# Kernel tuning notes

Hardware: AMD Instinct MI355X
Metric: run time of the kernel (lower is better)

## Reference

```python
import jax, jax.numpy as jnp
import numpy as np

B, S, D = 2, 2048, 1024   # batch, seq, d_model
L, H = 256, 512           # d_latent, d_hidden (expert MLP)
E = 8                     # num_experts
SH = 512                  # shared-expert hidden (= d_hidden)


def setup_inputs() -> dict:
    key = jax.random.key(0)
    ks = jax.random.split(key, 12)
    s = 0.02
    return {
        "x": jax.random.normal(ks[0], (B, S, D), dtype=jnp.float32),
        "w_router": jax.random.normal(ks[1], (E, D), dtype=jnp.float32) * s,
        "w_down": jax.random.normal(ks[2], (L, D), dtype=jnp.float32) * s,
        "w_up": jax.random.normal(ks[3], (D, L), dtype=jnp.float32) * s,
        "w1_e": jax.random.normal(ks[4], (E, H, L), dtype=jnp.float32) * s,
        "wg_e": jax.random.normal(ks[5], (E, H, L), dtype=jnp.float32) * s,
        "w2_e": jax.random.normal(ks[6], (E, L, H), dtype=jnp.float32) * s,
        "w1_s": jax.random.normal(ks[7], (SH, D), dtype=jnp.float32) * s,
        "wg_s": jax.random.normal(ks[8], (SH, D), dtype=jnp.float32) * s,
        "w2_s": jax.random.normal(ks[9], (D, SH), dtype=jnp.float32) * s,
        "top_k": 2,
    }


def reference(x, w_router, w_down, w_up, w1_e, wg_e, w2_e, w1_s, wg_s, w2_s, top_k):
    Bq, Sq, Dq = x.shape
    T = Bq * Sq
    xf = x.reshape(T, Dq)

    # --- router (fp32 logits, softmax over top-k values) ---
    logits = xf.astype(jnp.float32) @ w_router.T            # (T, E)
    topk_val, topk_idx = jax.lax.top_k(logits, top_k)       # (T, k)
    topk_w = jax.nn.softmax(topk_val, axis=-1).astype(x.dtype)
    # dense combine weights (T, E); zero for unselected experts
    comb = jnp.zeros((T, E), dtype=x.dtype)
    comb = comb.at[jnp.arange(T)[:, None], topk_idx].add(topk_w)

    # --- shared latent down-projection ---
    lat = xf @ w_down.T                                     # (T, L)

    # --- all-expert SwiGLU in latent space, then weighted combine ---
    g = jax.nn.silu(jnp.einsum('tl,ehl->teh', lat, wg_e))   # (T, E, H)
    a = jnp.einsum('tl,ehl->teh', lat, w1_e)                # (T, E, H)
    ex = jnp.einsum('teh,elh->tel', g * a, w2_e)            # (T, E, L)
    routed_lat = jnp.einsum('te,tel->tl', comb, ex)         # (T, L)
    routed = routed_lat @ w_up.T                            # (T, D)

    # --- shared (dense) SwiGLU expert in d_model ---
    shared = (jax.nn.silu(xf @ wg_s.T) * (xf @ w1_s.T)) @ w2_s.T

    y = routed + shared
    return y.reshape(Bq, Sq, Dq)
```

## Files before the change

kernel.cpp:

```cpp
#include <hip/hip_runtime.h>
#include <hip/hip_bf16.h>
#include <math.h>

#define T_TOK 4096
#define D_MODEL 1024
#define L_LAT 256
#define H_HID 512
#define E_EXP 8
#define SH_HID 512
#define TOT_EROWS (2 * T_TOK)

typedef __bf16 bf16x8 __attribute__((ext_vector_type(8)));
typedef float f32x4 __attribute__((ext_vector_type(4)));

__device__ __forceinline__ unsigned short f2bf(float f) {
    union { float f; unsigned int u; } c{f};
    unsigned int r = (c.u + 0x7fffu + ((c.u >> 16) & 1u)) >> 16;
    return (unsigned short)r;
}
__device__ __forceinline__ float bf2f(unsigned short u) {
    union { unsigned int u; float f; } c{(unsigned int)u << 16};
    return c.f;
}

__device__ __forceinline__ void gload_lds16(const unsigned short* g, unsigned short* l) {
    __builtin_amdgcn_global_load_lds(
        (const __attribute__((address_space(1))) void*)g,
        (__attribute__((address_space(3))) void*)l,
        16, 0, 0);
}

__device__ __forceinline__ int swz64(int row, int s) {
    return s ^ (row & 7);
}

__global__ __launch_bounds__(256)
void cast_router_kernel(const float* __restrict__ x, const float* __restrict__ w_router,
                        const float* __restrict__ w_down, const float* __restrict__ wg_s,
                        const float* __restrict__ w1_s,
                        unsigned short* __restrict__ xb, unsigned short* __restrict__ wdb,
                        unsigned short* __restrict__ wgsb, unsigned short* __restrict__ w1sb,
                        int* __restrict__ topk_idx, float* __restrict__ topk_w)
{
    __shared__ float wlds[E_EXP * D_MODEL];
    int bid = blockIdx.x;
    int tid = threadIdx.x;

    if (bid < 4096) {
        int j = (bid * 256 + tid) * 4;
        float4 v = *(const float4*)(x + j);
        ushort4 o = { f2bf(v.x), f2bf(v.y), f2bf(v.z), f2bf(v.w) };
        *(ushort4*)(xb + j) = o;
        return;
    }
    if (bid >= 5120) {
        int i = (bid - 5120) * 256 + tid;
        const float* src; unsigned short* dst; int base;
        if      (i < 65536)  { src = w_down; dst = wdb;  base = 0; }
        else if (i < 196608) { src = wg_s;   dst = wgsb; base = 65536; }
        else                 { src = w1_s;   dst = w1sb; base = 196608; }
        int j = (i - base) * 4;
        float4 v = *(const float4*)(src + j);
        ushort4 o = { f2bf(v.x), f2bf(v.y), f2bf(v.z), f2bf(v.w) };
        *(ushort4*)(dst + j) = o;
        return;
    }

    int rb = bid - 4096;
    for (int i = tid * 4; i < E_EXP * D_MODEL; i += 256 * 4)
        *(float4*)(wlds + i) = *(const float4*)(w_router + i);
    __syncthreads();

    int wid = tid >> 6, lane = tid & 63;
    int t = rb * 4 + wid;
    const float* xr = x + (size_t)t * D_MODEL;
    float acc[E_EXP];
#pragma unroll
    for (int e = 0; e < E_EXP; ++e) acc[e] = 0.f;
#pragma unroll 4
    for (int i = 0; i < D_MODEL / 64; ++i) {
        int d = lane + i * 64;
        float xv = xr[d];
#pragma unroll
        for (int e = 0; e < E_EXP; ++e)
            acc[e] = fmaf(xv, wlds[e * D_MODEL + d], acc[e]);
    }
#pragma unroll
    for (int e = 0; e < E_EXP; ++e)
        for (int off = 32; off > 0; off >>= 1)
            acc[e] += __shfl_xor(acc[e], off, 64);
    if (lane == 0) {
        int i0 = 0; float v0 = acc[0];
#pragma unroll
        for (int e = 1; e < E_EXP; ++e) if (acc[e] > v0) { v0 = acc[e]; i0 = e; }
        int i1 = -1; float v1 = -INFINITY;
#pragma unroll
        for (int e = 0; e < E_EXP; ++e) if (e != i0 && acc[e] > v1) { v1 = acc[e]; i1 = e; }
        float e1 = expf(v1 - v0);
        topk_idx[2 * t] = i0; topk_idx[2 * t + 1] = i1;
        topk_w[2 * t] = 1.f / (1.f + e1);
        topk_w[2 * t + 1] = e1 / (1.f + e1);
    }
}

__device__ void bucket_body(const int* __restrict__ topk_idx,
                            int* __restrict__ counts, int* __restrict__ offsets,
                            int* __restrict__ tok_of_row, int* __restrict__ row_of_pair,
                            int* sb)
{
    int* s_wavecnt  = sb;
    int* s_wavebase = sb + 32;
    int* s_tot      = sb + 64;
    int* s_off      = sb + 72;
    int tid = threadIdx.x, wave = tid >> 6, lane = tid & 63;
    int base_i = tid * 32;

    int cnt[E_EXP];
#pragma unroll
    for (int e = 0; e < E_EXP; ++e) cnt[e] = 0;
#pragma unroll
    for (int j = 0; j < 32; ++j) {
        int e = topk_idx[base_i + j];
#pragma unroll
        for (int q = 0; q < E_EXP; ++q) cnt[q] += (e == q) ? 1 : 0;
    }
    int excl[E_EXP];
#pragma unroll
    for (int e = 0; e < E_EXP; ++e) {
        int v = cnt[e];
#pragma unroll
        for (int off = 1; off < 64; off <<= 1) {
            int u = __shfl_up(v, off, 64);
            v += (lane >= off) ? u : 0;
        }
        excl[e] = v - cnt[e];
        if (lane == 63) s_wavecnt[wave * 8 + e] = v;
    }
    __syncthreads();
    if (tid < E_EXP) {
        int tot = 0;
        for (int w = 0; w < 4; ++w) tot += s_wavecnt[w * 8 + tid];
        s_tot[tid] = tot;
        counts[tid] = tot;
    }
    __syncthreads();
    if (tid == 0) {
        int off = 0;
        for (int e = 0; e < E_EXP; ++e) { s_off[e] = off; offsets[e] = off; off += s_tot[e]; }
    }
    __syncthreads();
    if (tid < E_EXP) {
        int run = s_off[tid];
        for (int w = 0; w < 4; ++w) { s_wavebase[w * 8 + tid] = run; run += s_wavecnt[w * 8 + tid]; }
    }
    __syncthreads();
    int tb[E_EXP];
#pragma unroll
    for (int e = 0; e < E_EXP; ++e) tb[e] = s_wavebase[wave * 8 + e] + excl[e];
#pragma unroll
    for (int j = 0; j < 32; ++j) {
        int item = base_i + j;
        int e = topk_idx[item];
        int p = 0;
#pragma unroll
        for (int q = 0; q < E_EXP; ++q) if (e == q) { p = tb[q]; tb[q] = p + 1; }
        tok_of_row[p] = item >> 1;
        row_of_pair[item] = p;
    }
}

template<bool DUAL, bool SILU, bool EXPERT, bool GATHER, int OUT_MODE>
__device__ void gemm_tile(unsigned short* As, unsigned short* Bs0, unsigned short* Bs1,
                          int m0, int n0, int e,
                          const unsigned short* __restrict__ A,
                          const unsigned short* __restrict__ B0g,
                          const unsigned short* __restrict__ B1g,
                          void* __restrict__ Cv,
                          int M, int K, int ldc,
                          const int* __restrict__ tok_of_row,
                          const int* __restrict__ offsets,
                          const int* __restrict__ counts,
                          long strideB)
{
    int m_base = EXPERT ? offsets[e] : 0;
    int m_count = EXPERT ? counts[e] : M;
    if (m0 >= m_count) return;

    const unsigned short* B0 = B0g + (EXPERT ? (size_t)e * strideB : 0);
    const unsigned short* B1 = DUAL ? (B1g + (EXPERT ? (size_t)e * strideB : 0)) : nullptr;

    int tid = threadIdx.x;
    int r8 = tid >> 3, slot = tid & 7;

    const unsigned short* aptr[4];
#pragma unroll
    for (int r = 0; r < 4; ++r) {
        int rl = r * 32 + r8;
        int mrow = m0 + rl;
        if (mrow >= m_count) mrow = m_count - 1;
        long grow;
        if (GATHER)      grow = tok_of_row[m_base + mrow];
        else if (EXPERT) grow = m_base + mrow;
        else             grow = mrow;
        aptr[r] = A + (size_t)grow * K + swz64(rl, slot) * 8;
    }
    const unsigned short* bptr0[2];
    const unsigned short* bptr1[2];
#pragma unroll
    for (int r = 0; r < 2; ++r) {
        int rl = r * 32 + r8;
        int gs = swz64(rl, slot) * 8;
        bptr0[r] = B0 + (size_t)(n0 + rl) * K + gs;
        if (DUAL) bptr1[r] = B1 + (size_t)(n0 + rl) * K + gs;
    }
    unsigned short* As_dst  = As  + tid * 8;
    unsigned short* Bs0_dst = Bs0 + tid * 8;
    unsigned short* Bs1_dst = DUAL ? (Bs1 + tid * 8) : nullptr;

    int wave = tid >> 6, lane = tid & 63;
    int wm0 = (wave >> 1) * 64, wn0 = (wave & 1) * 32;
    int l15 = lane & 15, kg = lane >> 4;

    f32x4 acc0[4][2] = {};
    f32x4 acc1[DUAL ? 4 : 1][DUAL ? 2 : 1] = {};

    for (int k0 = 0; k0 < K; k0 += 64) {
#pragma unroll
        for (int r = 0; r < 4; ++r)
            gload_lds16(aptr[r] + k0, As_dst + r * 2048);
#pragma unroll
        for (int r = 0; r < 2; ++r) {
            gload_lds16(bptr0[r] + k0, Bs0_dst + r * 2048);
            if constexpr (DUAL) gload_lds16(bptr1[r] + k0, Bs1_dst + r * 2048);
        }
        __syncthreads();

        bf16x8 af[2][4];
#pragma unroll
        for (int kh = 0; kh < 2; ++kh)
#pragma unroll
            for (int mf = 0; mf < 4; ++mf) {
                int row = wm0 + mf * 16 + l15;
                af[kh][mf] = *reinterpret_cast<const bf16x8*>(As + row * 64 + swz64(row, kh * 4 + kg) * 8);
            }
        bf16x8 bf0[2][2], bf1[2][2];
#pragma unroll
        for (int kh = 0; kh < 2; ++kh)
#pragma unroll
            for (int nf = 0; nf < 2; ++nf) {
                int row = wn0 + nf * 16 + l15;
                bf0[kh][nf] = *reinterpret_cast<const bf16x8*>(Bs0 + row * 64 + swz64(row, kh * 4 + kg) * 8);
                if constexpr (DUAL)
                    bf1[kh][nf] = *reinterpret_cast<const bf16x8*>(Bs1 + row * 64 + swz64(row, kh * 4 + kg) * 8);
            }
#pragma unroll
        for (int kh = 0; kh < 2; ++kh)
#pragma unroll
            for (int mf = 0; mf < 4; ++mf)
#pragma unroll
                for (int nf = 0; nf < 2; ++nf) {
                    acc0[mf][nf] = __builtin_amdgcn_mfma_f32_16x16x32_bf16(af[kh][mf], bf0[kh][nf], acc0[mf][nf], 0, 0, 0);
                    if constexpr (DUAL)
                        acc1[mf][nf] = __builtin_amdgcn_mfma_f32_16x16x32_bf16(af[kh][mf], bf1[kh][nf], acc1[mf][nf], 0, 0, 0);
                }
        __syncthreads();
    }

#pragma unroll
    for (int mf = 0; mf < 4; ++mf) {
#pragma unroll
        for (int r4 = 0; r4 < 4; ++r4) {
            int mrow = m0 + wm0 + mf * 16 + kg * 4 + r4;
            if (mrow >= m_count) continue;
            size_t crow = (size_t)((EXPERT ? m_base : 0) + mrow) * ldc + n0 + wn0;
#pragma unroll
            for (int nf = 0; nf < 2; ++nf) {
                float v = acc0[mf][nf][r4];
                if constexpr (SILU) {
                    float g = v;
                    float a = acc1[mf][nf][r4];
                    v = (g / (1.f + expf(-g))) * a;
                }
                int col = nf * 16 + l15;
                if constexpr (OUT_MODE == 1) ((unsigned short*)Cv)[crow + col] = f2bf(v);
                else                         ((float*)Cv)[crow + col] = v;
            }
        }
    }
}

template<bool EXPERT, int OUT_MODE, bool BLEND>
__device__ void gemm_tile_n128(unsigned short* SM,
                               int m0, int n0, int e,
                               const unsigned short* __restrict__ A,
                               const unsigned short* __restrict__ B0g,
                               void* __restrict__ Cv,
                               int M, int K, int ldc,
                               const int* __restrict__ offsets,
                               const int* __restrict__ counts,
                               long strideB,
                               const int* __restrict__ row_of_pair,
                               const float* __restrict__ topk_w)
{
    unsigned short* As = SM;
    unsigned short* Bs = SM + 128 * 64;

    int m_base = EXPERT ? offsets[e] : 0;
    int m_count = EXPERT ? counts[e] : M;
    if (m0 >= m_count) return;

    const unsigned short* B0 = B0g + (EXPERT ? (size_t)e * strideB : 0);

    int tid = threadIdx.x;
    int r8 = tid >> 3, slot = tid & 7;

    const unsigned short* aptr[4];
    const unsigned short* a2ptr[4];
    float wa[4], wb[4];
#pragma unroll
    for (int r = 0; r < 4; ++r) {
        int rl = r * 32 + r8;
        int mrow = m0 + rl;
        if (mrow >= m_count) mrow = m_count - 1;
        if constexpr (BLEND) {
            int t = m0 + rl;
            int rp0 = row_of_pair[2 * t], rp1 = row_of_pair[2 * t + 1];
            wa[r] = topk_w[2 * t]; wb[r] = topk_w[2 * t + 1];
            aptr[r]  = A + (size_t)rp0 * K + swz64(rl, slot) * 8;
            a2ptr[r] = A + (size_t)rp1 * K + swz64(rl, slot) * 8;
        } else {
            long grow = EXPERT ? (long)(m_base + mrow) : (long)mrow;
            aptr[r] = A + (size_t)grow * K + swz64(rl, slot) * 8;
        }
    }
    const unsigned short* bptr[4];
#pragma unroll
    for (int r = 0; r < 4; ++r) {
        int rl = r * 32 + r8;
        bptr[r] = B0 + (size_t)(n0 + rl) * K + swz64(rl, slot) * 8;
    }
    unsigned short* As_dst = As + tid * 8;
    unsigned short* Bs_dst = Bs + tid * 8;

    int wave = tid >> 6, lane = tid & 63;
    int wm0 = (wave >> 1) * 64, wn0 = (wave & 1) * 64;
    int l15 = lane & 15, kg = lane >> 4;

    f32x4 acc[4][4] = {};

    for (int k0 = 0; k0 < K; k0 += 64) {
        if constexpr (BLEND) {
#pragma unroll
            for (int r = 0; r < 4; ++r) {
                ushort4 u0 = *(const ushort4*)(aptr[r] + k0);
                ushort4 u1 = *(const ushort4*)(aptr[r] + k0 + 4);
                ushort4 v0 = *(const ushort4*)(a2ptr[r] + k0);
                ushort4 v1 = *(const ushort4*)(a2ptr[r] + k0 + 4);
                ushort4 lo = { f2bf(wa[r] * bf2f(u0.x) + wb[r] * bf2f(v0.x)),
                               f2bf(wa[r] * bf2f(u0.y) + wb[r] * bf2f(v0.y)),
                               f2bf(wa[r] * bf2f(u0.z) + wb[r] * bf2f(v0.z)),
                               f2bf(wa[r] * bf2f(u0.w) + wb[r] * bf2f(v0.w)) };
                ushort4 hi = { f2bf(wa[r] * bf2f(u1.x) + wb[r] * bf2f(v1.x)),
                               f2bf(wa[r] * bf2f(u1.y) + wb[r] * bf2f(v1.y)),
                               f2bf(wa[r] * bf2f(u1.z) + wb[r] * bf2f(v1.z)),
                               f2bf(wa[r] * bf2f(u1.w) + wb[r] * bf2f(v1.w)) };
                *(ushort4*)(As_dst + r * 2048) = lo;
                *(ushort4*)(As_dst + r * 2048 + 4) = hi;
                ushort4 b0 = *(const ushort4*)(bptr[r] + k0);
                ushort4 b1 = *(const ushort4*)(bptr[r] + k0 + 4);
                *(ushort4*)(Bs_dst + r * 2048) = b0;
                *(ushort4*)(Bs_dst + r * 2048 + 4) = b1;
            }
        } else {
#pragma unroll
            for (int r = 0; r < 4; ++r)
                gload_lds16(aptr[r] + k0, As_dst + r * 2048);
#pragma unroll
            for (int r = 0; r < 4; ++r)
                gload_lds16(bptr[r] + k0, Bs_dst + r * 2048);
        }
        __syncthreads();

        bf16x8 af[2][4], bfr[2][4];
#pragma unroll
        for (int kh = 0; kh < 2; ++kh) {
#pragma unroll
            for (int mf = 0; mf < 4; ++mf) {
                int row = wm0 + mf * 16 + l15;
                af[kh][mf] = *reinterpret_cast<const bf16x8*>(As + row * 64 + swz64(row, kh * 4 + kg) * 8);
            }
#pragma unroll
            for (int nf = 0; nf < 4; ++nf) {
                int row = wn0 + nf * 16 + l15;
                bfr[kh][nf] = *reinterpret_cast<const bf16x8*>(Bs + row * 64 + swz64(row, kh * 4 + kg) * 8);
            }
        }
#pragma unroll
        for (int kh = 0; kh < 2; ++kh)
#pragma unroll
            for (int mf = 0; mf < 4; ++mf)
#pragma unroll
                for (int nf = 0; nf < 4; ++nf)
                    acc[mf][nf] = __builtin_amdgcn_mfma_f32_16x16x32_bf16(af[kh][mf], bfr[kh][nf], acc[mf][nf], 0, 0, 0);
        __syncthreads();
    }

#pragma unroll
    for (int mf = 0; mf < 4; ++mf) {
#pragma unroll
        for (int r4 = 0; r4 < 4; ++r4) {
            int mrow = m0 + wm0 + mf * 16 + kg * 4 + r4;
            if (mrow >= m_count) continue;
            size_t crow = (size_t)((EXPERT ? m_base : 0) + mrow) * ldc + n0 + wn0;
#pragma unroll
            for (int nf = 0; nf < 4; ++nf) {
                float v = acc[mf][nf][r4];
                int col = nf * 16 + l15;
                if constexpr (OUT_MODE == 1)      ((unsigned short*)Cv)[crow + col] = f2bf(v);
                else if constexpr (OUT_MODE == 2) ((float*)Cv)[crow + col] += v;
                else                              ((float*)Cv)[crow + col] = v;
            }
        }
    }
}

__global__ __launch_bounds__(256)
void k_main(const unsigned short* __restrict__ x_bf,
            const unsigned short* __restrict__ wdown_bf,
            const unsigned short* __restrict__ wgs_bf,
            const unsigned short* __restrict__ w1s_bf,
            const float* __restrict__ wg_e, const float* __restrict__ w1_e,
            const float* __restrict__ w2_e,
            const float* __restrict__ w_up, const float* __restrict__ w2_s,
            unsigned short* __restrict__ lat_bf,
            unsigned short* __restrict__ hs,
            unsigned short* __restrict__ wge_bf, unsigned short* __restrict__ w1e_bf,
            unsigned short* __restrict__ w2e_bf, unsigned short* __restrict__ wup_bf,
            unsigned short* __restrict__ w2s_bf,
            const int* __restrict__ topk_idx,
            int* __restrict__ counts, int* __restrict__ offsets,
            int* __restrict__ tok_of_row, int* __restrict__ row_of_pair)
{
    __shared__ __align__(16) unsigned short SM[16384];
    unsigned short* As  = SM;
    unsigned short* Bs0 = SM + 8192;
    unsigned short* Bs1 = SM + 12288;

    int bid = blockIdx.x;
    int tid = threadIdx.x;

    if (bid == 384) {
        bucket_body(topk_idx, counts, offsets, tok_of_row, row_of_pair, (int*)SM);
        return;
    }
    if (bid > 384) {
        int i = (bid - 385) * 256 + tid;
        const float* src; unsigned short* dst; int base;
        if      (i < 262144) { src = wg_e; dst = wge_bf; base = 0; }
        else if (i < 524288) { src = w1_e; dst = w1e_bf; base = 262144; }
        else if (i < 786432) { src = w2_e; dst = w2e_bf; base = 524288; }
        else if (i < 851968) { src = w_up; dst = wup_bf; base = 786432; }
        else                 { src = w2_s; dst = w2s_bf; base = 851968; }
        int j = (i - base) * 4;
        float4 v = *(const float4*)(src + j);
        ushort4 o = { f2bf(v.x), f2bf(v.y), f2bf(v.z), f2bf(v.w) };
        *(ushort4*)(dst + j) = o;
        return;
    }

    int xq = bid & 31, y = bid >> 5;
    if (y < 4) {
        gemm_tile<false, false, false, false, 1>(As, Bs0, Bs1, xq * 128, y * 64, 0,
            x_bf, wdown_bf, nullptr, lat_bf, T_TOK, D_MODEL, L_LAT,
            nullptr, nullptr, nullptr, 0);
    } else {
        gemm_tile<true, true, false, false, 1>(As, Bs0, Bs1, xq * 128, (y - 4) * 64, 0,
            x_bf, wgs_bf, w1s_bf, hs, T_TOK, D_MODEL, SH_HID,
            nullptr, nullptr, nullptr, 0);
    }
}

__global__ __launch_bounds__(256)
void k_exp_sh(const unsigned short* __restrict__ lat_bf,
              const unsigned short* __restrict__ wge_bf,
              const unsigned short* __restrict__ w1e_bf,
              const unsigned short* __restrict__ hs,
              const unsigned short* __restrict__ w2s_bf,
              unsigned short* __restrict__ hbuf_bf,
              float* __restrict__ out,
              const int* __restrict__ tok_of_row,
              const int* __restrict__ offsets,
              const int* __restrict__ counts)
{
    __shared__ __align__(16) unsigned short SM[16384];
    int bid = blockIdx.x;
    if (bid < 4096) {
        int xq = bid >> 6, e = (bid >> 3) & 7, y = bid & 7;
        gemm_tile<true, true, true, true, 1>(SM, SM + 8192, SM + 12288,
            xq * 128, y * 64, e,
            lat_bf, wge_bf, w1e_bf, hbuf_bf, 0, L_LAT, H_HID,
            tok_of_row, offsets, counts, (long)H_HID * L_LAT);
    } else {
        int idx = bid - 4096;
        int xq = idx & 31, y = idx >> 5;
        gemm_tile_n128<false, 0, false>(SM, xq * 128, y * 128, 0,
            hs, w2s_bf, out, T_TOK, SH_HID, D_MODEL,
            nullptr, nullptr, 0, nullptr, nullptr);
    }
}

__global__ __launch_bounds__(256)
void k_expdown(const unsigned short* __restrict__ hbuf_bf,
               const unsigned short* __restrict__ w2e_bf,
               unsigned short* __restrict__ ex_bf,
               const int* __restrict__ offsets,
               const int* __restrict__ counts)
{
    __shared__ __align__(16) unsigned short SM[16384];
    gemm_tile_n128<true, 1, false>(SM,
        blockIdx.x * 128, blockIdx.y * 128, blockIdx.z,
        hbuf_bf, w2e_bf, ex_bf, 0, H_HID, L_LAT,
        offsets, counts, (long)L_LAT * H_HID, nullptr, nullptr);
}

__global__ __launch_bounds__(256)
void k_final(const unsigned short* __restrict__ ex_bf,
             const unsigned short* __restrict__ wup_bf,
             const int* __restrict__ row_of_pair,
             const float* __restrict__ topk_w,
             float* __restrict__ out)
{
    __shared__ __align__(16) unsigned short SM[16384];
    gemm_tile_n128<false, 2, true>(SM,
        blockIdx.x * 128, blockIdx.y * 128, 0,
        ex_bf, wup_bf, out, T_TOK, L_LAT, D_MODEL,
        nullptr, nullptr, 0, row_of_pair, topk_w);
}

extern "C" void kernel_launch(void* const* d_in, const int* in_sizes, int n_in,
                              void* d_out, int out_size, void* d_ws, size_t ws_size,
                              hipStream_t stream)
{
    const float* x        = (const float*)d_in[0];
    const float* w_router = (const float*)d_in[1];
    const float* w_down   = (const float*)d_in[2];
    const float* w_up     = (const float*)d_in[3];
    const float* w1_e     = (const float*)d_in[4];
    const float* wg_e     = (const float*)d_in[5];
    const float* w2_e     = (const float*)d_in[6];
    const float* w1_s     = (const float*)d_in[7];
    const float* wg_s     = (const float*)d_in[8];
    const float* w2_s     = (const float*)d_in[9];
    float* out = (float*)d_out;

    char* ws = (char*)d_ws;
    size_t off = 0;
    auto alloc = [&](size_t bytes) -> void* {
        void* p = ws + off;
        off += (bytes + 255) & ~(size_t)255;
        return p;
    };
    unsigned short* x_bf    = (unsigned short*)alloc((size_t)T_TOK * D_MODEL * 2);
    unsigned short* lat_bf  = (unsigned short*)alloc((size_t)T_TOK * L_LAT * 2);
    unsigned short* hs      = (unsigned short*)alloc((size_t)T_TOK * SH_HID * 2);
    unsigned short* ex_bf   = (unsigned short*)alloc((size_t)TOT_EROWS * L_LAT * 2);
    unsigned short* wdown_bf= (unsigned short*)alloc((size_t)L_LAT * D_MODEL * 2);
    unsigned short* wge_bf  = (unsigned short*)alloc((size_t)E_EXP * H_HID * L_LAT * 2);
    unsigned short* w1e_bf  = (unsigned short*)alloc((size_t)E_EXP * H_HID * L_LAT * 2);
    unsigned short* w2e_bf  = (unsigned short*)alloc((size_t)E_EXP * L_LAT * H_HID * 2);
    unsigned short* wgs_bf  = (unsigned short*)alloc((size_t)SH_HID * D_MODEL * 2);
    unsigned short* w1s_bf  = (unsigned short*)alloc((size_t)SH_HID * D_MODEL * 2);
    unsigned short* wup_bf  = (unsigned short*)alloc((size_t)D_MODEL * L_LAT * 2);
    unsigned short* w2s_bf  = (unsigned short*)alloc((size_t)D_MODEL * SH_HID * 2);
    int*   topk_idx    = (int*)alloc(T_TOK * 2 * 4);
    float* topk_w      = (float*)alloc(T_TOK * 2 * 4);
    int*   tok_of_row  = (int*)alloc(T_TOK * 2 * 4);
    int*   row_of_pair = (int*)alloc(T_TOK * 2 * 4);
    int*   counts      = (int*)alloc(E_EXP * 4);
    int*   offsets     = (int*)alloc(E_EXP * 4);
    unsigned short* hbuf_bf = x_bf;

    cast_router_kernel<<<6400, 256, 0, stream>>>(
        x, w_router, w_down, wg_s, w1_s,
        x_bf, wdown_bf, wgs_bf, w1s_bf, topk_idx, topk_w);

    k_main<<<4225, 256, 0, stream>>>(
        x_bf, wdown_bf, wgs_bf, w1s_bf, wg_e, w1_e, w2_e, w_up, w2_s,
        lat_bf, hs, wge_bf, w1e_bf, w2e_bf, wup_bf, w2s_bf,
        topk_idx, counts, offsets, tok_of_row, row_of_pair);

    k_exp_sh<<<4352, 256, 0, stream>>>(
        lat_bf, wge_bf, w1e_bf, hs, w2s_bf, hbuf_bf, out,
        tok_of_row, offsets, counts);

    k_expdown<<<dim3(TOT_EROWS / 128, L_LAT / 128, E_EXP), 256, 0, stream>>>(
        hbuf_bf, w2e_bf, ex_bf, offsets, counts);

    k_final<<<dim3(T_TOK / 128, D_MODEL / 128), 256, 0, stream>>>(
        ex_bf, wup_bf, row_of_pair, topk_w, out);
}
```

Before: 91.27 us.

## Store shared-expert output as bf16 and shrink N tiles for expert-down and final GEMMs

The shared-expert down GEMM now writes a bf16 scratch buffer instead of fp32 into the output. The final blended up-projection kernel reads that buffer and writes the output once, replacing the fp32 read-modify-write. The expert-down and final GEMMs switch from 128-wide to 64-wide N tiles, doubling block count for better occupancy and load balance on small grids. The cost is an extra bf16 rounding of the shared-expert contribution and more A-tile reloads per output column.

```diff
diff --git a/kernel.cpp b/kernel.cpp
--- a/kernel.cpp
+++ b/kernel.cpp
@@ -289,7 +289,7 @@
     }
 }
 
-template<bool EXPERT, int OUT_MODE, bool BLEND>
+template<bool EXPERT, int OUT_MODE>
 __device__ void gemm_tile_n128(unsigned short* SM,
                                int m0, int n0, int e,
                                const unsigned short* __restrict__ A,
@@ -298,9 +298,7 @@
                                int M, int K, int ldc,
                                const int* __restrict__ offsets,
                                const int* __restrict__ counts,
-                               long strideB,
-                               const int* __restrict__ row_of_pair,
-                               const float* __restrict__ topk_w)
+                               long strideB)
 {
     unsigned short* As = SM;
     unsigned short* Bs = SM + 128 * 64;
@@ -315,23 +313,13 @@
     int r8 = tid >> 3, slot = tid & 7;
 
     const unsigned short* aptr[4];
-    const unsigned short* a2ptr[4];
-    float wa[4], wb[4];
 #pragma unroll
     for (int r = 0; r < 4; ++r) {
         int rl = r * 32 + r8;
         int mrow = m0 + rl;
         if (mrow >= m_count) mrow = m_count - 1;
-        if constexpr (BLEND) {
-            int t = m0 + rl;
-            int rp0 = row_of_pair[2 * t], rp1 = row_of_pair[2 * t + 1];
-            wa[r] = topk_w[2 * t]; wb[r] = topk_w[2 * t + 1];
-            aptr[r]  = A + (size_t)rp0 * K + swz64(rl, slot) * 8;
-            a2ptr[r] = A + (size_t)rp1 * K + swz64(rl, slot) * 8;
-        } else {
-            long grow = EXPERT ? (long)(m_base + mrow) : (long)mrow;
-            aptr[r] = A + (size_t)grow * K + swz64(rl, slot) * 8;
-        }
+        long grow = EXPERT ? (long)(m_base + mrow) : (long)mrow;
+        aptr[r] = A + (size_t)grow * K + swz64(rl, slot) * 8;
     }
     const unsigned short* bptr[4];
 #pragma unroll
@@ -349,36 +337,12 @@
     f32x4 acc[4][4] = {};
 
     for (int k0 = 0; k0 < K; k0 += 64) {
-        if constexpr (BLEND) {
-#pragma unroll
-            for (int r = 0; r < 4; ++r) {
-                ushort4 u0 = *(const ushort4*)(aptr[r] + k0);
-                ushort4 u1 = *(const ushort4*)(aptr[r] + k0 + 4);
-                ushort4 v0 = *(const ushort4*)(a2ptr[r] + k0);
-                ushort4 v1 = *(const ushort4*)(a2ptr[r] + k0 + 4);
-                ushort4 lo = { f2bf(wa[r] * bf2f(u0.x) + wb[r] * bf2f(v0.x)),
-                               f2bf(wa[r] * bf2f(u0.y) + wb[r] * bf2f(v0.y)),
-                               f2bf(wa[r] * bf2f(u0.z) + wb[r] * bf2f(v0.z)),
-                               f2bf(wa[r] * bf2f(u0.w) + wb[r] * bf2f(v0.w)) };
-                ushort4 hi = { f2bf(wa[r] * bf2f(u1.x) + wb[r] * bf2f(v1.x)),
-                               f2bf(wa[r] * bf2f(u1.y) + wb[r] * bf2f(v1.y)),
-                               f2bf(wa[r] * bf2f(u1.z) + wb[r] * bf2f(v1.z)),
-                               f2bf(wa[r] * bf2f(u1.w) + wb[r] * bf2f(v1.w)) };
-                *(ushort4*)(As_dst + r * 2048) = lo;
-                *(ushort4*)(As_dst + r * 2048 + 4) = hi;
-                ushort4 b0 = *(const ushort4*)(bptr[r] + k0);
-                ushort4 b1 = *(const ushort4*)(bptr[r] + k0 + 4);
-                *(ushort4*)(Bs_dst + r * 2048) = b0;
-                *(ushort4*)(Bs_dst + r * 2048 + 4) = b1;
-            }
-        } else {
-#pragma unroll
-            for (int r = 0; r < 4; ++r)
-                gload_lds16(aptr[r] + k0, As_dst + r * 2048);
-#pragma unroll
-            for (int r = 0; r < 4; ++r)
-                gload_lds16(bptr[r] + k0, Bs_dst + r * 2048);
-        }
+#pragma unroll
+        for (int r = 0; r < 4; ++r)
+            gload_lds16(aptr[r] + k0, As_dst + r * 2048);
+#pragma unroll
+        for (int r = 0; r < 4; ++r)
+            gload_lds16(bptr[r] + k0, Bs_dst + r * 2048);
         __syncthreads();
 
         bf16x8 af[2][4], bfr[2][4];
@@ -416,9 +380,8 @@
             for (int nf = 0; nf < 4; ++nf) {
                 float v = acc[mf][nf][r4];
                 int col = nf * 16 + l15;
-                if constexpr (OUT_MODE == 1)      ((unsigned short*)Cv)[crow + col] = f2bf(v);
-                else if constexpr (OUT_MODE == 2) ((float*)Cv)[crow + col] += v;
-                else                              ((float*)Cv)[crow + col] = v;
+                if constexpr (OUT_MODE == 1) ((unsigned short*)Cv)[crow + col] = f2bf(v);
+                else                         ((float*)Cv)[crow + col] = v;
             }
         }
     }
@@ -487,7 +450,7 @@
               const unsigned short* __restrict__ hs,
               const unsigned short* __restrict__ w2s_bf,
               unsigned short* __restrict__ hbuf_bf,
-              float* __restrict__ out,
+              unsigned short* __restrict__ outs,
               const int* __restrict__ tok_of_row,
               const int* __restrict__ offsets,
               const int* __restrict__ counts)
@@ -503,9 +466,9 @@
     } else {
         int idx = bid - 4096;
         int xq = idx & 31, y = idx >> 5;
-        gemm_tile_n128<false, 0, false>(SM, xq * 128, y * 128, 0,
-            hs, w2s_bf, out, T_TOK, SH_HID, D_MODEL,
-            nullptr, nullptr, 0, nullptr, nullptr);
+        gemm_tile_n128<false, 1>(SM, xq * 128, y * 128, 0,
+            hs, w2s_bf, outs, T_TOK, SH_HID, D_MODEL,
+            nullptr, nullptr, 0);
     }
 }
 
@@ -517,24 +480,114 @@
                const int* __restrict__ counts)
 {
     __shared__ __align__(16) unsigned short SM[16384];
-    gemm_tile_n128<true, 1, false>(SM,
-        blockIdx.x * 128, blockIdx.y * 128, blockIdx.z,
-        hbuf_bf, w2e_bf, ex_bf, 0, H_HID, L_LAT,
-        offsets, counts, (long)L_LAT * H_HID, nullptr, nullptr);
+    gemm_tile<false, false, true, false, 1>(SM, SM + 8192, SM + 12288,
+        blockIdx.x * 128, blockIdx.y * 64, blockIdx.z,
+        hbuf_bf, w2e_bf, nullptr, ex_bf, 0, H_HID, L_LAT,
+        nullptr, offsets, counts, (long)L_LAT * H_HID);
 }
 
 __global__ __launch_bounds__(256)
 void k_final(const unsigned short* __restrict__ ex_bf,
              const unsigned short* __restrict__ wup_bf,
+             const unsigned short* __restrict__ outs,
              const int* __restrict__ row_of_pair,
              const float* __restrict__ topk_w,
              float* __restrict__ out)
 {
-    __shared__ __align__(16) unsigned short SM[16384];
-    gemm_tile_n128<false, 2, true>(SM,
-        blockIdx.x * 128, blockIdx.y * 128, 0,
-        ex_bf, wup_bf, out, T_TOK, L_LAT, D_MODEL,
-        nullptr, nullptr, 0, row_of_pair, topk_w);
+    __shared__ __align__(16) unsigned short As[128 * 64];
+    __shared__ __align__(16) unsigned short Bs[64 * 64];
+
+    int m0 = blockIdx.x * 128, n0 = blockIdx.y * 64;
+    int tid = threadIdx.x;
+    int r8 = tid >> 3, slot = tid & 7;
+
+    const unsigned short* aptr[4];
+    const unsigned short* a2ptr[4];
+    float wa[4], wb[4];
+#pragma unroll
+    for (int r = 0; r < 4; ++r) {
+        int rl = r * 32 + r8;
+        int t = m0 + rl;
+        int rp0 = row_of_pair[2 * t], rp1 = row_of_pair[2 * t + 1];
+        wa[r] = topk_w[2 * t]; wb[r] = topk_w[2 * t + 1];
+        int gs = swz64(rl, slot) * 8;
+        aptr[r]  = ex_bf + (size_t)rp0 * L_LAT + gs;
+        a2ptr[r] = ex_bf + (size_t)rp1 * L_LAT + gs;
+    }
+    const unsigned short* bptr[2];
+#pragma unroll
+    for (int r = 0; r < 2; ++r) {
+        int rl = r * 32 + r8;
+        bptr[r] = wup_bf + (size_t)(n0 + rl) * L_LAT + swz64(rl, slot) * 8;
+    }
+    unsigned short* As_dst = As + tid * 8;
+    unsigned short* Bs_dst = Bs + tid * 8;
+
+    int wave = tid >> 6, lane = tid & 63;
+    int wm0 = (wave >> 1) * 64, wn0 = (wave & 1) * 32;
+    int l15 = lane & 15, kg = lane >> 4;
+
+    f32x4 acc[4][2] = {};
+
+    for (int k0 = 0; k0 < L_LAT; k0 += 64) {
+#pragma unroll
+        for (int r = 0; r < 4; ++r) {
+            ushort4 u0 = *(const ushort4*)(aptr[r] + k0);
+            ushort4 u1 = *(const ushort4*)(aptr[r] + k0 + 4);
+            ushort4 v0 = *(const ushort4*)(a2ptr[r] + k0);
+            ushort4 v1 = *(const ushort4*)(a2ptr[r] + k0 + 4);
+            ushort4 lo = { f2bf(wa[r] * bf2f(u0.x) + wb[r] * bf2f(v0.x)),
+                           f2bf(wa[r] * bf2f(u0.y) + wb[r] * bf2f(v0.y)),
+                           f2bf(wa[r] * bf2f(u0.z) + wb[r] * bf2f(v0.z)),
+                           f2bf(wa[r] * bf2f(u0.w) + wb[r] * bf2f(v0.w)) };
+            ushort4 hi = { f2bf(wa[r] * bf2f(u1.x) + wb[r] * bf2f(v1.x)),
+                           f2bf(wa[r] * bf2f(u1.y) + wb[r] * bf2f(v1.y)),
+                           f2bf(wa[r] * bf2f(u1.z) + wb[r] * bf2f(v1.z)),
+                           f2bf(wa[r] * bf2f(u1.w) + wb[r] * bf2f(v1.w)) };
+            *(ushort4*)(As_dst + r * 2048) = lo;
+            *(ushort4*)(As_dst + r * 2048 + 4) = hi;
+        }
+#pragma unroll
+        for (int r = 0; r < 2; ++r)
+            gload_lds16(bptr[r] + k0, Bs_dst + r * 2048);
+        __syncthreads();
+
+        bf16x8 af[2][4], bfr[2][2];
+#pragma unroll
+        for (int kh = 0; kh < 2; ++kh) {
+#pragma unroll
+            for (int mf = 0; mf < 4; ++mf) {
+                int row = wm0 + mf * 16 + l15;
+                af[kh][mf] = *reinterpret_cast<const bf16x8*>(As + row * 64 + swz64(row, kh * 4 + kg) * 8);
+            }
+#pragma unroll
+            for (int nf = 0; nf < 2; ++nf) {
+                int row = wn0 + nf * 16 + l15;
+                bfr[kh][nf] = *reinterpret_cast<const bf16x8*>(Bs + row * 64 + swz64(row, kh * 4 + kg) * 8);
+            }
+        }
+#pragma unroll
+        for (int kh = 0; kh < 2; ++kh)
+#pragma unroll
+            for (int mf = 0; mf < 4; ++mf)
+#pragma unroll
+                for (int nf = 0; nf < 2; ++nf)
+                    acc[mf][nf] = __builtin_amdgcn_mfma_f32_16x16x32_bf16(af[kh][mf], bfr[kh][nf], acc[mf][nf], 0, 0, 0);
+        __syncthreads();
+    }
+
+#pragma unroll
+    for (int mf = 0; mf < 4; ++mf)
+#pragma unroll
+        for (int r4 = 0; r4 < 4; ++r4) {
+            int mrow = m0 + wm0 + mf * 16 + kg * 4 + r4;
+            size_t crow = (size_t)mrow * D_MODEL + n0 + wn0;
+#pragma unroll
+            for (int nf = 0; nf < 2; ++nf) {
+                int col = nf * 16 + l15;
+                out[crow + col] = acc[mf][nf][r4] + bf2f(outs[crow + col]);
+            }
+        }
 }
 
 extern "C" void kernel_launch(void* const* d_in, const int* in_sizes, int n_in,
@@ -563,6 +616,7 @@
     unsigned short* x_bf    = (unsigned short*)alloc((size_t)T_TOK * D_MODEL * 2);
     unsigned short* lat_bf  = (unsigned short*)alloc((size_t)T_TOK * L_LAT * 2);
     unsigned short* hs      = (unsigned short*)alloc((size_t)T_TOK * SH_HID * 2);
+    unsigned short* outs    = (unsigned short*)alloc((size_t)T_TOK * D_MODEL * 2);
     unsigned short* ex_bf   = (unsigned short*)alloc((size_t)TOT_EROWS * L_LAT * 2);
     unsigned short* wdown_bf= (unsigned short*)alloc((size_t)L_LAT * D_MODEL * 2);
     unsigned short* wge_bf  = (unsigned short*)alloc((size_t)E_EXP * H_HID * L_LAT * 2);
@@ -590,12 +644,12 @@
         topk_idx, counts, offsets, tok_of_row, row_of_pair);
 
     k_exp_sh<<<4352, 256, 0, stream>>>(
-        lat_bf, wge_bf, w1e_bf, hs, w2s_bf, hbuf_bf, out,
+        lat_bf, wge_bf, w1e_bf, hs, w2s_bf, hbuf_bf, outs,
         tok_of_row, offsets, counts);
 
-    k_expdown<<<dim3(TOT_EROWS / 128, L_LAT / 128, E_EXP), 256, 0, stream>>>(
+    k_expdown<<<dim3(TOT_EROWS / 128, L_LAT / 64, E_EXP), 256, 0, stream>>>(
         hbuf_bf, w2e_bf, ex_bf, offsets, counts);
 
-    k_final<<<dim3(T_TOK / 128, D_MODEL / 128), 256, 0, stream>>>(
-        ex_bf, wup_bf, row_of_pair, topk_w, out);
-}
+    k_final<<<dim3(T_TOK / 128, D_MODEL / 64), 256, 0, stream>>>(
+        ex_bf, wup_bf, outs, row_of_pair, topk_w, out);
+}
```

Measured after the change: 85.07 us. -6.8%, faster.
